# Optimization experiments

Measured on AMD Instinct MI355X. Metric: run time of the kernel, lower is better.

The kernel has to match this reference:

```python
import jax, jax.numpy as jnp
import numpy as np

N_WIDTH = 8
N_ORDER = 2
N_ELEMENTS = 1024
N_NODES = N_ELEMENTS * N_ORDER + 1  # 2049
N_SAMPLES = 4096
X_MIN = 0.0
X_MAX = 1.0


def _ref_nodes():
    return np.linspace(-1.0, 1.0, N_ORDER + 1)


def _lagrange(x):
    # x: [I, K] -> [I, K, P]
    nodes = _ref_nodes()
    cols = []
    for j in range(N_ORDER + 1):
        p = jnp.ones_like(x)
        for m in range(N_ORDER + 1):
            if j != m:
                p = p * (x - nodes[m]) / (nodes[j] - nodes[m])
        cols.append(p)
    return jnp.stack(cols, axis=-1)


def _dlagrange(x):
    nodes = _ref_nodes()
    cols = []
    for j in range(N_ORDER + 1):
        y = jnp.zeros_like(x)
        for i in range(N_ORDER + 1):
            if i != j:
                k = jnp.ones_like(x) / (nodes[j] - nodes[i])
                for m in range(N_ORDER + 1):
                    if m != i and m != j:
                        k = k * (x - nodes[m]) / (nodes[j] - nodes[m])
                y = y + k
        cols.append(y)
    return jnp.stack(cols, axis=-1)


def _ddlagrange(x):
    nodes = _ref_nodes()
    cols = []
    for j in range(N_ORDER + 1):
        y = jnp.zeros_like(x)
        for i in range(N_ORDER + 1):
            if i != j:
                k_sum = jnp.zeros_like(x)
                for m in range(N_ORDER + 1):
                    if m != i and m != j:
                        k_prod = jnp.ones_like(x) / (nodes[j] - nodes[m])
                        for n in range(N_ORDER + 1):
                            if n != i and n != j and n != m:
                                k_prod = k_prod * (x - nodes[n]) / (nodes[j] - nodes[n])
                        k_sum = k_sum + k_prod
                y = y + (1.0 / (nodes[j] - nodes[i])) * k_sum
        cols.append(y)
    return jnp.stack(cols, axis=-1)


def setup_inputs() -> dict:
    key = jax.random.key(0)
    k1, k2 = jax.random.split(key)
    x = jax.random.uniform(k1, (N_SAMPLES,), dtype=jnp.float32)  # in [x_min, x_max)
    weight = jax.random.normal(k2, (N_WIDTH, N_NODES), dtype=jnp.float32) * 0.02
    return {"x": x, "weight": weight}


def reference(x, weight):
    # replicate 1-D input across width: [I] -> [I, K]
    x2 = jnp.repeat(x[:, None], N_WIDTH, axis=-1)
    x_shift = (N_NODES - 1) * (x2 - X_MIN) / (X_MAX - X_MIN)
    id_el = jnp.clip(jnp.floor(x_shift / N_ORDER), 0, N_ELEMENTS - 1)
    nodes_l = (id_el * N_ORDER).astype(jnp.int32)  # [I, K]
    nodes_lf = jax.lax.stop_gradient(nodes_l.astype(x_shift.dtype))
    # reference coord: (x_shift - 0.5*(l + r)) / (0.5*(r - l)) with r = l + n_order
    x_t = (x_shift - (nodes_lf + 0.5 * N_ORDER)) / (0.5 * N_ORDER)

    delta_x = 0.5 * N_ORDER * (X_MAX - X_MIN) / (N_NODES - 1)
    phi_loc = _lagrange(x_t)                       # [I, K, P]
    dphi_loc = _dlagrange(x_t) / delta_x
    ddphi_loc = _ddlagrange(x_t) / (delta_x * delta_x)

    I, K = x2.shape
    P = N_ORDER + 1
    idx = nodes_l[:, :, None] + jnp.arange(P)      # [I, K, P] global node ids
    ii = jnp.arange(I)[:, None, None]
    kk = jnp.arange(K)[None, :, None]
    phi_ikp = jnp.zeros((I, K, N_NODES), x2.dtype).at[ii, kk, idx].set(phi_loc)
    dphi_ikp = jnp.zeros((I, K, N_NODES), x2.dtype).at[ii, kk, idx].set(dphi_loc)
    ddphi_ikp = jnp.zeros((I, K, N_NODES), x2.dtype).at[ii, kk, idx].set(ddphi_loc)

    t_ik = jnp.einsum('kp,ikp->ik', weight, phi_ikp)
    dt_ik = jnp.einsum('kp,ikp->ik', weight, dphi_ikp)
    ddt_ik = jnp.einsum('kp,ikp->ik', weight, ddphi_ikp)
    return (t_ik, dt_ik, ddt_ik, phi_ikp, dphi_ikp, ddphi_ikp)
```

## Files before the change

kernel.cpp:

```cpp
#include <hip/hip_runtime.h>


#define KN_NODES    2049
#define KN_SAMPLES  4096
#define KN_IK       (KN_SAMPLES * 8)
#define KN_HEAD     (3 * KN_IK)
#define KN_PHI_LEN  ((size_t)KN_IK * KN_NODES)

__device__ __forceinline__ void kann_coord(float xv, int& nl, float& x_t) {
    float xs  = 2048.0f * xv;
    float fid = floorf(0.5f * xs);
    fid = fminf(fmaxf(fid, 0.0f), 1023.0f);
    nl  = 2 * (int)fid;
    x_t = xs - (float)nl - 1.0f;
}

__global__ __launch_bounds__(256)
void KANN_scatter(const float* __restrict__ x, const float* __restrict__ w,
                  float* __restrict__ out) {
    int t = blockIdx.x * 256 + threadIdx.x;

    if (t < KN_IK) {
        int ik = t;
        int i = ik >> 3, k = ik & 7;
        int nl; float x_t; kann_coord(x[i], nl, x_t);
        const float* wk = w + k * KN_NODES + nl;
        float w0 = wk[0], w1 = wk[1], w2 = wk[2];
        float p0 = 0.5f * x_t * (x_t - 1.0f);
        float p1 = 1.0f - x_t * x_t;
        float p2 = 0.5f * x_t * (x_t + 1.0f);
        out[ik]             = w0 * p0 + w1 * p1 + w2 * p2;
        out[KN_IK + ik]     = (w0 * (x_t - 0.5f) - 2.0f * w1 * x_t + w2 * (x_t + 0.5f)) * 2048.0f;
        out[2 * KN_IK + ik] = (w0 - 2.0f * w1 + w2) * 4194304.0f;
    } else {
        int s = t - KN_IK;
        if (s >= 3 * KN_IK) return;
        int y  = s >> 15;
        int ik = s & (KN_IK - 1);
        int i  = ik >> 3;
        int nl; float x_t; kann_coord(x[i], nl, x_t);
        float b0, b1, b2;
        if (y == 0)      { b0 = 0.5f * x_t * (x_t - 1.0f); b1 = 1.0f - x_t * x_t; b2 = 0.5f * x_t * (x_t + 1.0f); }
        else if (y == 1) { b0 = (x_t - 0.5f) * 2048.0f; b1 = -4096.0f * x_t; b2 = (x_t + 0.5f) * 2048.0f; }
        else             { b0 = 4194304.0f; b1 = -8388608.0f; b2 = 4194304.0f; }
        float* p = out + KN_HEAD + (size_t)y * KN_PHI_LEN + (size_t)ik * KN_NODES + nl;
        p[0] = b0; p[1] = b1; p[2] = b2;
    }
}

extern "C" void kernel_launch(void* const* d_in, const int* in_sizes, int n_in,
                              void* d_out, int out_size, void* d_ws, size_t ws_size,
                              hipStream_t stream) {
    const float* x = (const float*)d_in[0];
    const float* w = (const float*)d_in[1];
    float* out = (float*)d_out;

    hipMemsetAsync(out, 0, (size_t)out_size * sizeof(float), stream);

    const int total = 4 * KN_IK;
    KANN_scatter<<<dim3(total / 256), dim3(256), 0, stream>>>(x, w, out);
}
```

Measured before the change: 151.7 us.

## Replace memset plus sparse scatter with dense fill kernel writing zeros and basis values

Drops the full-output memset and the scattered three-value writes. A small pre-kernel now computes the heads and a per-sample (node, local coord) table, and a dense fill kernel writes every element of the three phi planes exactly once: the basis value at the three active columns and zero everywhere else. The aim is to avoid a second pass over the large output (memset followed by scatter) and to make the writes coalesced across columns. The cost is a second launch, a workspace table, and per-element select logic.

```diff
diff --git a/kernel.cpp b/kernel.cpp
--- a/kernel.cpp
+++ b/kernel.cpp
@@ -7,44 +7,60 @@
 #define KN_HEAD     (3 * KN_IK)
 #define KN_PHI_LEN  ((size_t)KN_IK * KN_NODES)
 
-__device__ __forceinline__ void kann_coord(float xv, int& nl, float& x_t) {
+__global__ __launch_bounds__(256)
+void KANN_pre(const float* __restrict__ x, const float* __restrict__ w,
+              float* __restrict__ out, int2* __restrict__ tbl) {
+    int ik = blockIdx.x * 256 + threadIdx.x;
+    if (ik >= KN_IK) return;
+    int i = ik >> 3, k = ik & 7;
+    float xv  = x[i];
     float xs  = 2048.0f * xv;
     float fid = floorf(0.5f * xs);
     fid = fminf(fmaxf(fid, 0.0f), 1023.0f);
-    nl  = 2 * (int)fid;
-    x_t = xs - (float)nl - 1.0f;
+    int   nl  = 2 * (int)fid;
+    float x_t = xs - (float)nl - 1.0f;
+    if (k == 0) tbl[i] = make_int2(nl, __float_as_int(x_t));
+
+    const float* wk = w + k * KN_NODES + nl;
+    float w0 = wk[0], w1 = wk[1], w2 = wk[2];
+    float p0 = 0.5f * x_t * (x_t - 1.0f);
+    float p1 = 1.0f - x_t * x_t;
+    float p2 = 0.5f * x_t * (x_t + 1.0f);
+    out[ik]             = w0 * p0 + w1 * p1 + w2 * p2;
+    out[KN_IK + ik]     = (w0 * (x_t - 0.5f) - 2.0f * w1 * x_t + w2 * (x_t + 0.5f)) * 2048.0f;
+    out[2 * KN_IK + ik] = (w0 - 2.0f * w1 + w2) * 4194304.0f;
 }
 
 __global__ __launch_bounds__(256)
-void KANN_scatter(const float* __restrict__ x, const float* __restrict__ w,
-                  float* __restrict__ out) {
-    int t = blockIdx.x * 256 + threadIdx.x;
+void KANN_fill(const int2* __restrict__ tbl, float* __restrict__ out) {
+    const int c     = blockIdx.x * 256 + threadIdx.x;
+    const int plane = blockIdx.z;
+    const int rbase = blockIdx.y * 128;
+    const bool cv   = (c < KN_NODES);
 
-    if (t < KN_IK) {
-        int ik = t;
-        int i = ik >> 3, k = ik & 7;
-        int nl; float x_t; kann_coord(x[i], nl, x_t);
-        const float* wk = w + k * KN_NODES + nl;
-        float w0 = wk[0], w1 = wk[1], w2 = wk[2];
-        float p0 = 0.5f * x_t * (x_t - 1.0f);
-        float p1 = 1.0f - x_t * x_t;
-        float p2 = 0.5f * x_t * (x_t + 1.0f);
-        out[ik]             = w0 * p0 + w1 * p1 + w2 * p2;
-        out[KN_IK + ik]     = (w0 * (x_t - 0.5f) - 2.0f * w1 * x_t + w2 * (x_t + 0.5f)) * 2048.0f;
-        out[2 * KN_IK + ik] = (w0 - 2.0f * w1 + w2) * 4194304.0f;
-    } else {
-        int s = t - KN_IK;
-        if (s >= 3 * KN_IK) return;
-        int y  = s >> 15;
-        int ik = s & (KN_IK - 1);
-        int i  = ik >> 3;
-        int nl; float x_t; kann_coord(x[i], nl, x_t);
+    float* base = out + KN_HEAD + (size_t)plane * KN_PHI_LEN
+                + (size_t)rbase * KN_NODES + c;
+
+#pragma unroll
+    for (int r8 = 0; r8 < 16; ++r8) {
+        int2 e   = tbl[blockIdx.y * 16 + r8];
+        int   nl = e.x;
+        float xt = __int_as_float(e.y);
+
         float b0, b1, b2;
-        if (y == 0)      { b0 = 0.5f * x_t * (x_t - 1.0f); b1 = 1.0f - x_t * x_t; b2 = 0.5f * x_t * (x_t + 1.0f); }
-        else if (y == 1) { b0 = (x_t - 0.5f) * 2048.0f; b1 = -4096.0f * x_t; b2 = (x_t + 0.5f) * 2048.0f; }
-        else             { b0 = 4194304.0f; b1 = -8388608.0f; b2 = 4194304.0f; }
-        float* p = out + KN_HEAD + (size_t)y * KN_PHI_LEN + (size_t)ik * KN_NODES + nl;
-        p[0] = b0; p[1] = b1; p[2] = b2;
+        if (plane == 0)      { b0 = 0.5f * xt * (xt - 1.0f); b1 = 1.0f - xt * xt; b2 = 0.5f * xt * (xt + 1.0f); }
+        else if (plane == 1) { b0 = (xt - 0.5f) * 2048.0f; b1 = -4096.0f * xt; b2 = (xt + 0.5f) * 2048.0f; }
+        else                 { b0 = 4194304.0f; b1 = -8388608.0f; b2 = 4194304.0f; }
+
+        int   d = c - nl;
+        float v = (d == 0) ? b0 : ((d == 1) ? b1 : ((d == 2) ? b2 : 0.0f));
+
+        if (cv) {
+            float* p = base + (size_t)(r8 * 8) * KN_NODES;
+#pragma unroll
+            for (int j = 0; j < 8; ++j)
+                p[(size_t)j * KN_NODES] = v;
+        }
     }
 }
 
@@ -54,9 +70,8 @@
     const float* x = (const float*)d_in[0];
     const float* w = (const float*)d_in[1];
     float* out = (float*)d_out;
+    int2* tbl = (int2*)d_ws;
 
-    hipMemsetAsync(out, 0, (size_t)out_size * sizeof(float), stream);
-
-    const int total = 4 * KN_IK;
-    KANN_scatter<<<dim3(total / 256), dim3(256), 0, stream>>>(x, w, out);
+    KANN_pre<<<dim3(KN_IK / 256), dim3(256), 0, stream>>>(x, w, out, tbl);
+    KANN_fill<<<dim3(9, 256, 3), dim3(256), 0, stream>>>(tbl, out);
 }
```

New measurement: 298.7 us. 96.9% more time.
